# Performance work log

Hardware: AMD Instinct MI355X
Metric: run time of the kernel (lower is better)

Reference implementation:

```python
import jax, jax.numpy as jnp
import numpy as np

N_NODES = 70839  # num_user + num_item from config
N_EDGES = 2_000_000
EMB_DIM = 64
EPS = 1e-12  # torch F.normalize default eps


def setup_inputs() -> dict:
    key = jax.random.key(0)
    k1, k2, k3, k4 = jax.random.split(key, 4)
    ego_embedding = jax.random.normal(k1, (N_NODES, EMB_DIM), dtype=jnp.float32)
    edge_weight = jax.random.uniform(k2, (N_EDGES,), dtype=jnp.float32)
    edge_src = jax.random.randint(k3, (N_EDGES,), 0, N_NODES, dtype=jnp.int32)
    edge_dst = jax.random.randint(k4, (N_EDGES,), 0, N_NODES, dtype=jnp.int32)
    return {
        "ego_embedding": ego_embedding,
        "edge_weight": edge_weight,
        "edge_src": edge_src,
        "edge_dst": edge_dst,
    }


def reference(ego_embedding, edge_weight, edge_src, edge_dst):
    # message: m_e = h[src_e] * w_e   (u_mul_e)
    m = ego_embedding[edge_src] * edge_weight[:, None]          # [E, D]
    # reduce: h_v = sum_{e: dst_e = v} m_e   (fn.sum)
    h = jax.ops.segment_sum(m, edge_dst, num_segments=N_NODES)  # [N, D]
    # F.normalize(h, dim=1, p=2): x / max(||x||_2, eps)
    norm = jnp.linalg.norm(h, axis=1, keepdims=True)
    return h / jnp.maximum(norm, EPS)
```

## Files before the change

### kernel.cpp

```cpp
#include <hip/hip_runtime.h>
#include <hip/hip_fp16.h>

#define EMB_D 64
#define SB 1024
#define SPAN 128
#define MAXG 1024
#define NCHUNK2 512
#define CHMAX 4096
#define TILE 4096
#define CAST_BLOCKS 256


__device__ __forceinline__ float h15_to_float(unsigned int bits) {
    return __half2float(__ushort_as_half((unsigned short)bits));
}

__global__ void a1_cast_hist(const float2* __restrict__ embin,
                             __half2* __restrict__ emb16, int n2,
                             const int* __restrict__ dst,
                             int* __restrict__ cntT,
                             int E, int G, int chunk) {
    if (blockIdx.x < CAST_BLOCKS) {
        int i = blockIdx.x * blockDim.x + threadIdx.x;
        int st = CAST_BLOCKS * blockDim.x;
        for (; i < n2; i += st)
            emb16[i] = __float22half2_rn(embin[i]);
    } else {
        __shared__ int bins[MAXG];
        int hb = blockIdx.x - CAST_BLOCKS;
        for (int g = threadIdx.x; g < G; g += blockDim.x) bins[g] = 0;
        __syncthreads();
        int beg = hb * chunk;
        int end = min(beg + chunk, E);
        for (int i = beg + threadIdx.x; i < end; i += blockDim.x)
            atomicAdd(&bins[dst[i] >> 7], 1);
        __syncthreads();
        for (int g = threadIdx.x; g < G; g += blockDim.x)
            cntT[g * NCHUNK2 + hb] = bins[g];
    }
}

__global__ void scan_reduceB(const int* __restrict__ counts,
                             int* __restrict__ partial, int M) {
    __shared__ int wsum[16];
    const int tid = threadIdx.x, lane = tid & 63, wid = tid >> 6;
    int i = blockIdx.x * SB + tid;
    int v = (i < M) ? counts[i] : 0;
    #pragma unroll
    for (int off = 32; off > 0; off >>= 1)
        v += __shfl_xor(v, off, 64);
    if (lane == 0) wsum[wid] = v;
    __syncthreads();
    if (tid == 0) {
        int s = 0;
        #pragma unroll
        for (int k = 0; k < 16; ++k) s += wsum[k];
        partial[blockIdx.x] = s;
    }
}

__global__ void scan_partials(const int* __restrict__ partial,
                              int* __restrict__ blockoff,
                              int* __restrict__ offsets, int numB, int M) {
    __shared__ int wsum[16];
    __shared__ int wpre[16];
    __shared__ int carry;
    const int tid = threadIdx.x, lane = tid & 63, wid = tid >> 6;
    if (tid == 0) carry = 0;
    const int nPass = (numB + SB - 1) / SB;
    for (int p = 0; p < nPass; ++p) {
        __syncthreads();
        int base = carry;
        int idx = p * SB + tid;
        int v = (idx < numB) ? partial[idx] : 0;
        int x = v;
        #pragma unroll
        for (int off = 1; off < 64; off <<= 1) {
            int t = __shfl_up(x, off, 64);
            if (lane >= off) x += t;
        }
        if (lane == 63) wsum[wid] = x;
        __syncthreads();
        if (wid == 0) {
            int s = (lane < 16) ? wsum[lane] : 0;
            #pragma unroll
            for (int off = 1; off < 16; off <<= 1) {
                int t = __shfl_up(s, off, 64);
                if (lane >= off) s += t;
            }
            if (lane < 16) wpre[lane] = s;
        }
        __syncthreads();
        int excl = base + ((wid > 0) ? wpre[wid - 1] : 0) + (x - v);
        if (idx < numB) blockoff[idx] = excl;
        __syncthreads();
        if (tid == 0) carry = base + wpre[15];
    }
    __syncthreads();
    if (tid == 0) offsets[M] = carry;
}

__global__ void scan_applyB(const int* __restrict__ counts,
                            const int* __restrict__ blockoff,
                            int* __restrict__ offsets, int M) {
    __shared__ int wsum[16];
    __shared__ int wpre[16];
    const int tid = threadIdx.x, lane = tid & 63, wid = tid >> 6;
    int i = blockIdx.x * SB + tid;
    int v = (i < M) ? counts[i] : 0;
    int x = v;
    #pragma unroll
    for (int off = 1; off < 64; off <<= 1) {
        int t = __shfl_up(x, off, 64);
        if (lane >= off) x += t;
    }
    if (lane == 63) wsum[wid] = x;
    __syncthreads();
    if (wid == 0) {
        int s = (lane < 16) ? wsum[lane] : 0;
        #pragma unroll
        for (int off = 1; off < 16; off <<= 1) {
            int t = __shfl_up(s, off, 64);
            if (lane >= off) s += t;
        }
        if (lane < 16) wpre[lane] = s;
    }
    __syncthreads();
    int excl = blockoff[blockIdx.x] + ((wid > 0) ? wpre[wid - 1] : 0) + (x - v);
    if (i < M) offsets[i] = excl;
}

__global__ __launch_bounds__(256) void partition_sort(
        const int* __restrict__ src,
        const int* __restrict__ dst,
        const float* __restrict__ w,
        const int* __restrict__ cntT,
        const int* __restrict__ scanT,
        uint2* __restrict__ stream8,
        int E, int G, int chunk) {
    __shared__ uint2 recs[CHMAX];
    __shared__ int cur[MAXG];
    __shared__ int delta[MAXG];
    __shared__ int wtot[4];

    const int tid = threadIdx.x, lane = tid & 63, wv = tid >> 6;
    const int b = blockIdx.x;
    const int beg = b * chunk;
    const int end = min(beg + chunk, E);
    const int n = end - beg;

    const int K = (G + 255) >> 8;
    int vals[4];
    int acc = 0;
    #pragma unroll
    for (int k = 0; k < 4; ++k) {
        int g = tid * K + k;
        int c = (k < K && g < G) ? cntT[g * NCHUNK2 + b] : 0;
        vals[k] = c;
        acc += c;
    }
    int x = acc;
    #pragma unroll
    for (int off = 1; off < 64; off <<= 1) {
        int t = __shfl_up(x, off, 64);
        if (lane >= off) x += t;
    }
    if (lane == 63) wtot[wv] = x;
    __syncthreads();
    int woff = 0;
    #pragma unroll
    for (int k2 = 0; k2 < 4; ++k2)
        woff += (k2 < wv) ? wtot[k2] : 0;
    int run = woff + x - acc;
    #pragma unroll
    for (int k = 0; k < 4; ++k) {
        int g = tid * K + k;
        if (k < K && g < G) {
            cur[g] = run;
            delta[g] = scanT[g * NCHUNK2 + b] - run;
            run += vals[k];
        }
    }
    __syncthreads();

    for (int i = beg + tid; i < end; i += blockDim.x) {
        int d = dst[i];
        unsigned int wb = __half_as_ushort(__float2half_rn(w[i]));
        unsigned int pk = ((unsigned int)src[i] << 15) | (wb & 0x7FFFu);
        int g = d >> 7;
        int j = atomicAdd(&cur[g], 1);
        recs[j] = make_uint2(pk, (unsigned int)(d & (SPAN - 1)) |
                                 ((unsigned int)g << 7));
    }
    __syncthreads();

    for (int j = tid; j < n; j += blockDim.x) {
        uint2 r = recs[j];
        int g = (int)(r.y >> 7);
        stream8[delta[g] + j] = make_uint2(r.x, r.y & (SPAN - 1u));
    }
}

__global__ __launch_bounds__(512) void gather_fused(
        const char* __restrict__ emb16b,
        const uint2* __restrict__ stream8,
        const int* __restrict__ scanT,
        float* __restrict__ out, int N) {
    __shared__ uint2 lrec[TILE];
    __shared__ unsigned int srt[TILE];
    __shared__ int hcnt[SPAN];
    __shared__ int nstart[SPAN];
    __shared__ int cur[SPAN];
    __shared__ int wtot[2];

    const int g = blockIdx.x;
    const int tid = threadIdx.x;
    const int lane = tid & 63, wv = tid >> 6;
    const int base = scanT[g * NCHUNK2];
    const int endE = scanT[(g + 1) * NCHUNK2];
    const int crew = tid >> 4;
    const int ql = tid & 15;
    const unsigned qlo = (unsigned)(ql << 3);

    float4 acc[4];
    #pragma unroll
    for (int ni = 0; ni < 4; ++ni) acc[ni] = make_float4(0.f, 0.f, 0.f, 0.f);

    for (int tb = base; tb < endE; tb += TILE) {
        const int n = min(TILE, endE - tb);
        if (tid < SPAN) hcnt[tid] = 0;
        __syncthreads();
        for (int j = tid; j < n; j += 512) {
            uint2 r = stream8[tb + j];
            lrec[j] = r;
            atomicAdd(&hcnt[r.y], 1);
        }
        __syncthreads();
        int v = (tid < SPAN) ? hcnt[tid] : 0;
        int x = v;
        #pragma unroll
        for (int off = 1; off < 64; off <<= 1) {
            int t = __shfl_up(x, off, 64);
            if (lane >= off) x += t;
        }
        if (wv < 2 && lane == 63) wtot[wv] = x;
        __syncthreads();
        if (tid < SPAN) {
            int excl = x - v + ((wv == 1) ? wtot[0] : 0);
            nstart[tid] = excl;
            cur[tid] = excl;
        }
        __syncthreads();
        for (int j = tid; j < n; j += 512) {
            uint2 r = lrec[j];
            int slot = atomicAdd(&cur[r.y], 1);
            srt[slot] = r.x;
        }
        __syncthreads();
        #pragma unroll
        for (int ni = 0; ni < 4; ++ni) {
            int nd = crew + (ni << 5);
            int s = nstart[nd];
            int e = cur[nd];
            float4 a = acc[ni];
            unsigned int pk0 = (s < e) ? srt[s] : 0u;
            uint2 r0 = *reinterpret_cast<const uint2*>(
                emb16b + ((pk0 >> 15) * 128u + qlo));
            for (int k = s; k < e; ++k) {
                unsigned int pk1 = (k + 1 < e) ? srt[k + 1] : 0u;
                uint2 r1 = *reinterpret_cast<const uint2*>(
                    emb16b + ((pk1 >> 15) * 128u + qlo));
                float wt = h15_to_float(pk0 & 0x7FFFu);
                float2 x01 = __half22float2(*reinterpret_cast<__half2*>(&r0.x));
                float2 x23 = __half22float2(*reinterpret_cast<__half2*>(&r0.y));
                a.x = fmaf(x01.x, wt, a.x);
                a.y = fmaf(x01.y, wt, a.y);
                a.z = fmaf(x23.x, wt, a.z);
                a.w = fmaf(x23.y, wt, a.w);
                pk0 = pk1; r0 = r1;
            }
            acc[ni] = a;
        }
        __syncthreads();
    }

    #pragma unroll
    for (int ni = 0; ni < 4; ++ni) {
        int node = g * SPAN + crew + (ni << 5);
        float4 a = acc[ni];
        float ss = a.x * a.x + a.y * a.y + a.z * a.z + a.w * a.w;
        ss += __shfl_xor(ss, 1, 64);
        ss += __shfl_xor(ss, 2, 64);
        ss += __shfl_xor(ss, 4, 64);
        ss += __shfl_xor(ss, 8, 64);
        float scale = 1.0f / fmaxf(sqrtf(ss), 1e-12f);
        if (node < N) {
            float4 o = make_float4(a.x * scale, a.y * scale,
                                   a.z * scale, a.w * scale);
            *reinterpret_cast<float4*>(out + (size_t)node * EMB_D
                                       + (ql << 2)) = o;
        }
    }
}

__global__ void group_csr2(const uint2* __restrict__ stream8,
                           const int* __restrict__ scanT,
                           unsigned int* __restrict__ packed,
                           int* __restrict__ offsets, int N, int E) {
    __shared__ int hcnt[SPAN];
    __shared__ int cur[SPAN];
    __shared__ int wtot[4];
    int g = blockIdx.x;
    int tid = threadIdx.x;
    int base = scanT[g * NCHUNK2];
    int endE = scanT[(g + 1) * NCHUNK2];
    if (tid < SPAN) hcnt[tid] = 0;
    __syncthreads();
    for (int i = base + tid; i < endE; i += blockDim.x)
        atomicAdd(&hcnt[stream8[i].y], 1);
    __syncthreads();
    int v = (tid < SPAN) ? hcnt[tid] : 0;
    int lane = tid & 63, wv = tid >> 6;
    int x = v;
    #pragma unroll
    for (int off = 1; off < 64; off <<= 1) {
        int t = __shfl_up(x, off, 64);
        if (lane >= off) x += t;
    }
    if (lane == 63) wtot[wv] = x;
    __syncthreads();
    if (tid < SPAN) {
        int excl = x - v + ((wv == 1) ? wtot[0] : 0);
        cur[tid] = base + excl;
        int node = g * SPAN + tid;
        if (node < N) offsets[node] = base + excl;
    }
    if (g == 0 && tid == 0) offsets[N] = E;
    __syncthreads();
    for (int i = base + tid; i < endE; i += blockDim.x) {
        uint2 r = stream8[i];
        int slot = atomicAdd(&cur[r.y], 1);
        packed[slot] = r.x;
    }
}

__global__ __launch_bounds__(256) void gatherV_kernel(
        const char* __restrict__ emb16b,
        const int* __restrict__ offsets,
        const unsigned int* __restrict__ packed,
        float* __restrict__ out, int N) {
    int node = blockIdx.x * 4 + (threadIdx.x >> 6);
    int lane = threadIdx.x & 63;
    if (node >= N) return;
    int q  = lane >> 3;
    int ql = lane & 7;
    const unsigned qlo = (unsigned)(ql << 4);

    int beg = offsets[node];
    int end = offsets[node + 1];

    float a0=0.f,a1=0.f,a2=0.f,a3=0.f,a4=0.f,a5=0.f,a6=0.f,a7=0.f;

    int idx0 = beg + q;
    int idx1 = idx0 + 8;
    int idx2 = idx1 + 8;
    unsigned int pk0 = (idx0 < end) ? packed[idx0] : 0u;
    unsigned int pk1 = (idx1 < end) ? packed[idx1] : 0u;
    unsigned int pk2 = (idx2 < end) ? packed[idx2] : 0u;
    uint4 r0 = *reinterpret_cast<const uint4*>(emb16b + ((pk0 >> 15) * 128u + qlo));
    uint4 r1 = *reinterpret_cast<const uint4*>(emb16b + ((pk1 >> 15) * 128u + qlo));

    for (int j = beg; j < end; j += 8) {
        uint4 r2 = *reinterpret_cast<const uint4*>(
            emb16b + ((pk2 >> 15) * 128u + qlo));
        int idx3 = idx2 + 8;
        unsigned int pk3 = (idx3 < end) ? packed[idx3] : 0u;

        float wt = h15_to_float(pk0 & 0x7FFFu);
        float2 x01 = __half22float2(*reinterpret_cast<__half2*>(&r0.x));
        float2 x23 = __half22float2(*reinterpret_cast<__half2*>(&r0.y));
        float2 x45 = __half22float2(*reinterpret_cast<__half2*>(&r0.z));
        float2 x67 = __half22float2(*reinterpret_cast<__half2*>(&r0.w));
        a0 = fmaf(x01.x, wt, a0);
        a1 = fmaf(x01.y, wt, a1);
        a2 = fmaf(x23.x, wt, a2);
        a3 = fmaf(x23.y, wt, a3);
        a4 = fmaf(x45.x, wt, a4);
        a5 = fmaf(x45.y, wt, a5);
        a6 = fmaf(x67.x, wt, a6);
        a7 = fmaf(x67.y, wt, a7);

        pk0 = pk1; pk1 = pk2; pk2 = pk3;
        r0 = r1; r1 = r2;
        idx2 = idx3;
    }

    #pragma unroll
    for (int off = 8; off < 64; off <<= 1) {
        a0 += __shfl_xor(a0, off, 64);
        a1 += __shfl_xor(a1, off, 64);
        a2 += __shfl_xor(a2, off, 64);
        a3 += __shfl_xor(a3, off, 64);
        a4 += __shfl_xor(a4, off, 64);
        a5 += __shfl_xor(a5, off, 64);
        a6 += __shfl_xor(a6, off, 64);
        a7 += __shfl_xor(a7, off, 64);
    }
    float ss = a0*a0 + a1*a1 + a2*a2 + a3*a3 + a4*a4 + a5*a5 + a6*a6 + a7*a7;
    ss += __shfl_xor(ss, 1, 64);
    ss += __shfl_xor(ss, 2, 64);
    ss += __shfl_xor(ss, 4, 64);
    float scale = 1.0f / fmaxf(sqrtf(ss), 1e-12f);

    if (q == 0) {
        float4* po = reinterpret_cast<float4*>(out + (size_t)node * EMB_D
                                               + (ql << 3));
        po[0] = make_float4(a0 * scale, a1 * scale, a2 * scale, a3 * scale);
        po[1] = make_float4(a4 * scale, a5 * scale, a6 * scale, a7 * scale);
    }
}

__global__ void lightgcn_scatter(const float* __restrict__ emb,
                                 const float* __restrict__ w,
                                 const int* __restrict__ src,
                                 const int* __restrict__ dst,
                                 float* __restrict__ h, int E) {
    long long t = (long long)blockIdx.x * blockDim.x + threadIdx.x;
    int e = (int)(t >> 4);
    int d = (int)(t & 15) << 2;
    if (e >= E) return;
    int s = src[e]; int v = dst[e]; float wt = w[e];
    const float4 m = *reinterpret_cast<const float4*>(emb + (size_t)s * EMB_D + d);
    float* o = h + (size_t)v * EMB_D + d;
    unsafeAtomicAdd(o + 0, m.x * wt);
    unsafeAtomicAdd(o + 1, m.y * wt);
    unsafeAtomicAdd(o + 2, m.z * wt);
    unsafeAtomicAdd(o + 3, m.w * wt);
}

__global__ void lightgcn_normalize(float* __restrict__ h, int N) {
    int row = blockIdx.x * (blockDim.x >> 6) + (threadIdx.x >> 6);
    int lane = threadIdx.x & 63;
    if (row >= N) return;
    float x = h[(size_t)row * EMB_D + lane];
    float ss = x * x;
    #pragma unroll
    for (int off = 32; off > 0; off >>= 1)
        ss += __shfl_xor(ss, off, 64);
    h[(size_t)row * EMB_D + lane] = x / fmaxf(sqrtf(ss), 1e-12f);
}

extern "C" void kernel_launch(void* const* d_in, const int* in_sizes, int n_in,
                              void* d_out, int out_size, void* d_ws, size_t ws_size,
                              hipStream_t stream) {
    const float* emb = (const float*)d_in[0];
    const float* w   = (const float*)d_in[1];
    const int*   src = (const int*)d_in[2];
    const int*   dst = (const int*)d_in[3];
    float* out = (float*)d_out;

    const int N = in_sizes[0] / EMB_D;
    const int E = in_sizes[1];
    const int block = 256;
    const int G = (N + SPAN - 1) / SPAN;

    const int M3 = G * NCHUNK2;
    const int numB3 = (M3 + SB - 1) / SB;
    const int chunk3 = (E + NCHUNK2 - 1) / NCHUNK2;

    size_t intsA5 = (size_t)M3 + (size_t)(M3 + 1) + 2 * (size_t)numB3;
    size_t strOff5 = (intsA5 * sizeof(int) + 15) & ~(size_t)15;
    size_t embOff5 = (strOff5 + (size_t)E * sizeof(uint2) + 15) & ~(size_t)15;
    size_t neededA5 = embOff5 + (size_t)N * EMB_D * sizeof(__half);

    size_t intsA3 = (size_t)M3 + (size_t)(M3 + 1) + 2 * (size_t)numB3
                  + (size_t)(N + 1);
    size_t strOff = (intsA3 * sizeof(int) + 15) & ~(size_t)15;
    size_t pkdOff = strOff + (size_t)E * sizeof(uint2);
    size_t embOff3 = (pkdOff + (size_t)E * sizeof(unsigned int) + 15)
                     & ~(size_t)15;
    size_t neededA3 = embOff3 + (size_t)N * EMB_D * sizeof(__half);

    if (ws_size >= neededA5 && G <= MAXG && chunk3 <= CHMAX &&
        E < (1 << 28) && N < (1 << 17)) {
        int* cntT     = (int*)d_ws;
        int* scanT    = cntT + M3;
        int* partial  = scanT + M3 + 1;
        int* blockoff = partial + numB3;
        uint2* stream8 = (uint2*)((char*)d_ws + strOff5);
        __half2* emb16 = (__half2*)((char*)d_ws + embOff5);

        int n2 = N * (EMB_D / 2);

        a1_cast_hist<<<CAST_BLOCKS + NCHUNK2, block, 0, stream>>>(
            (const float2*)emb, emb16, n2, dst, cntT, E, G, chunk3);

        scan_reduceB<<<numB3, SB, 0, stream>>>(cntT, partial, M3);
        scan_partials<<<1, SB, 0, stream>>>(partial, blockoff, scanT, numB3, M3);
        scan_applyB<<<numB3, SB, 0, stream>>>(cntT, blockoff, scanT, M3);

        partition_sort<<<NCHUNK2, block, 0, stream>>>(src, dst, w, cntT, scanT,
                                                      stream8, E, G, chunk3);

        gather_fused<<<G, 512, 0, stream>>>((const char*)emb16, stream8,
                                            scanT, out, N);
    } else if (ws_size >= neededA3 && G <= MAXG && chunk3 <= CHMAX &&
               E < (1 << 28) && N < (1 << 17)) {
        int* cntT     = (int*)d_ws;
        int* scanT    = cntT + M3;
        int* partial  = scanT + M3 + 1;
        int* blockoff = partial + numB3;
        int* offsets  = blockoff + numB3;
        uint2* stream8 = (uint2*)((char*)d_ws + strOff);
        unsigned int* packed = (unsigned int*)((char*)d_ws + pkdOff);
        __half2* emb16 = (__half2*)((char*)d_ws + embOff3);

        int n2 = N * (EMB_D / 2);

        a1_cast_hist<<<CAST_BLOCKS + NCHUNK2, block, 0, stream>>>(
            (const float2*)emb, emb16, n2, dst, cntT, E, G, chunk3);

        scan_reduceB<<<numB3, SB, 0, stream>>>(cntT, partial, M3);
        scan_partials<<<1, SB, 0, stream>>>(partial, blockoff, scanT, numB3, M3);
        scan_applyB<<<numB3, SB, 0, stream>>>(cntT, blockoff, scanT, M3);

        partition_sort<<<NCHUNK2, block, 0, stream>>>(src, dst, w, cntT, scanT,
                                                      stream8, E, G, chunk3);
        group_csr2<<<G, block, 0, stream>>>(stream8, scanT, packed, offsets,
                                            N, E);

        int gridN = (N + 3) / 4;
        gatherV_kernel<<<gridN, 256, 0, stream>>>((const char*)emb16, offsets,
                                                  packed, out, N);
    } else {
        hipMemsetAsync(d_out, 0, (size_t)out_size * sizeof(float), stream);
        long long total = (long long)E * 16;
        int grid = (int)((total + block - 1) / block);
        lightgcn_scatter<<<grid, block, 0, stream>>>(emb, w, src, dst, out, E);
        int gridN = (N + 3) / 4;
        lightgcn_normalize<<<gridN, 256, 0, stream>>>(out, N);
    }
}
```

Measured before the change: 191.1 us.

## Split gather edge loop across two half-crews with 16-byte loads; widen partition_sort blocks

In the fused gather, each 16-lane node crew is split into two 8-lane halves. Each half handles alternate edges and loads 8 fp16 values (16 bytes) per lane instead of 4. The two partial sums are merged with an xor-8 shuffle before normalization. This aims to halve the serial per-node edge loop length and make wider memory transactions, at the cost of doubled accumulator registers and extra shuffles. Separately, partition_sort is launched with 512 threads instead of 256 to add parallelism during the scatter into shared memory.

Result: faster. 175.4 us (-8.2%).

```diff
diff --git a/kernel.cpp b/kernel.cpp
--- a/kernel.cpp
+++ b/kernel.cpp
@@ -130,7 +130,7 @@
     if (i < M) offsets[i] = excl;
 }
 
-__global__ __launch_bounds__(256) void partition_sort(
+__global__ __launch_bounds__(512) void partition_sort(
         const int* __restrict__ src,
         const int* __restrict__ dst,
         const float* __restrict__ w,
@@ -141,7 +141,7 @@
     __shared__ uint2 recs[CHMAX];
     __shared__ int cur[MAXG];
     __shared__ int delta[MAXG];
-    __shared__ int wtot[4];
+    __shared__ int wtot[8];
 
     const int tid = threadIdx.x, lane = tid & 63, wv = tid >> 6;
     const int b = blockIdx.x;
@@ -149,11 +149,11 @@
     const int end = min(beg + chunk, E);
     const int n = end - beg;
 
-    const int K = (G + 255) >> 8;
-    int vals[4];
+    const int K = (G + 511) >> 9;
+    int vals[2];
     int acc = 0;
     #pragma unroll
-    for (int k = 0; k < 4; ++k) {
+    for (int k = 0; k < 2; ++k) {
         int g = tid * K + k;
         int c = (k < K && g < G) ? cntT[g * NCHUNK2 + b] : 0;
         vals[k] = c;
@@ -169,11 +169,11 @@
     __syncthreads();
     int woff = 0;
     #pragma unroll
-    for (int k2 = 0; k2 < 4; ++k2)
+    for (int k2 = 0; k2 < 8; ++k2)
         woff += (k2 < wv) ? wtot[k2] : 0;
     int run = woff + x - acc;
     #pragma unroll
-    for (int k = 0; k < 4; ++k) {
+    for (int k = 0; k < 2; ++k) {
         int g = tid * K + k;
         if (k < K && g < G) {
             cur[g] = run;
@@ -183,7 +183,7 @@
     }
     __syncthreads();
 
-    for (int i = beg + tid; i < end; i += blockDim.x) {
+    for (int i = beg + tid; i < end; i += 512) {
         int d = dst[i];
         unsigned int wb = __half_as_ushort(__float2half_rn(w[i]));
         unsigned int pk = ((unsigned int)src[i] << 15) | (wb & 0x7FFFu);
@@ -194,7 +194,7 @@
     }
     __syncthreads();
 
-    for (int j = tid; j < n; j += blockDim.x) {
+    for (int j = tid; j < n; j += 512) {
         uint2 r = recs[j];
         int g = (int)(r.y >> 7);
         stream8[delta[g] + j] = make_uint2(r.x, r.y & (SPAN - 1u));
@@ -220,11 +220,16 @@
     const int endE = scanT[(g + 1) * NCHUNK2];
     const int crew = tid >> 4;
     const int ql = tid & 15;
-    const unsigned qlo = (unsigned)(ql << 3);
-
-    float4 acc[4];
-    #pragma unroll
-    for (int ni = 0; ni < 4; ++ni) acc[ni] = make_float4(0.f, 0.f, 0.f, 0.f);
+    const int sub = ql >> 3;
+    const int sl = ql & 7;
+    const unsigned qlo = (unsigned)(sl << 4);
+
+    float4 accA[4], accB[4];
+    #pragma unroll
+    for (int ni = 0; ni < 4; ++ni) {
+        accA[ni] = make_float4(0.f, 0.f, 0.f, 0.f);
+        accB[ni] = make_float4(0.f, 0.f, 0.f, 0.f);
+    }
 
     for (int tb = base; tb < endE; tb += TILE) {
         const int n = min(TILE, endE - tb);
@@ -262,43 +267,63 @@
             int nd = crew + (ni << 5);
             int s = nstart[nd];
             int e = cur[nd];
-            float4 a = acc[ni];
-            unsigned int pk0 = (s < e) ? srt[s] : 0u;
-            uint2 r0 = *reinterpret_cast<const uint2*>(
+            float4 aA = accA[ni];
+            float4 aB = accB[ni];
+            int k0 = s + sub;
+            unsigned int pk0 = (k0 < e) ? srt[k0] : 0u;
+            uint4 r0 = *reinterpret_cast<const uint4*>(
                 emb16b + ((pk0 >> 15) * 128u + qlo));
-            for (int k = s; k < e; ++k) {
-                unsigned int pk1 = (k + 1 < e) ? srt[k + 1] : 0u;
-                uint2 r1 = *reinterpret_cast<const uint2*>(
+            for (int k = k0; k < e; k += 2) {
+                int k1 = k + 2;
+                unsigned int pk1 = (k1 < e) ? srt[k1] : 0u;
+                uint4 r1 = *reinterpret_cast<const uint4*>(
                     emb16b + ((pk1 >> 15) * 128u + qlo));
                 float wt = h15_to_float(pk0 & 0x7FFFu);
                 float2 x01 = __half22float2(*reinterpret_cast<__half2*>(&r0.x));
                 float2 x23 = __half22float2(*reinterpret_cast<__half2*>(&r0.y));
-                a.x = fmaf(x01.x, wt, a.x);
-                a.y = fmaf(x01.y, wt, a.y);
-                a.z = fmaf(x23.x, wt, a.z);
-                a.w = fmaf(x23.y, wt, a.w);
+                float2 x45 = __half22float2(*reinterpret_cast<__half2*>(&r0.z));
+                float2 x67 = __half22float2(*reinterpret_cast<__half2*>(&r0.w));
+                aA.x = fmaf(x01.x, wt, aA.x);
+                aA.y = fmaf(x01.y, wt, aA.y);
+                aA.z = fmaf(x23.x, wt, aA.z);
+                aA.w = fmaf(x23.y, wt, aA.w);
+                aB.x = fmaf(x45.x, wt, aB.x);
+                aB.y = fmaf(x45.y, wt, aB.y);
+                aB.z = fmaf(x67.x, wt, aB.z);
+                aB.w = fmaf(x67.y, wt, aB.w);
                 pk0 = pk1; r0 = r1;
             }
-            acc[ni] = a;
+            accA[ni] = aA;
+            accB[ni] = aB;
         }
         __syncthreads();
     }
 
     #pragma unroll
     for (int ni = 0; ni < 4; ++ni) {
+        accA[ni].x += __shfl_xor(accA[ni].x, 8, 64);
+        accA[ni].y += __shfl_xor(accA[ni].y, 8, 64);
+        accA[ni].z += __shfl_xor(accA[ni].z, 8, 64);
+        accA[ni].w += __shfl_xor(accA[ni].w, 8, 64);
+        accB[ni].x += __shfl_xor(accB[ni].x, 8, 64);
+        accB[ni].y += __shfl_xor(accB[ni].y, 8, 64);
+        accB[ni].z += __shfl_xor(accB[ni].z, 8, 64);
+        accB[ni].w += __shfl_xor(accB[ni].w, 8, 64);
         int node = g * SPAN + crew + (ni << 5);
-        float4 a = acc[ni];
-        float ss = a.x * a.x + a.y * a.y + a.z * a.z + a.w * a.w;
+        float4 aA = accA[ni];
+        float4 aB = accB[ni];
+        float ss = aA.x * aA.x + aA.y * aA.y + aA.z * aA.z + aA.w * aA.w
+                 + aB.x * aB.x + aB.y * aB.y + aB.z * aB.z + aB.w * aB.w;
         ss += __shfl_xor(ss, 1, 64);
         ss += __shfl_xor(ss, 2, 64);
         ss += __shfl_xor(ss, 4, 64);
-        ss += __shfl_xor(ss, 8, 64);
         float scale = 1.0f / fmaxf(sqrtf(ss), 1e-12f);
         if (node < N) {
+            float4 a = sub ? aB : aA;
             float4 o = make_float4(a.x * scale, a.y * scale,
                                    a.z * scale, a.w * scale);
             *reinterpret_cast<float4*>(out + (size_t)node * EMB_D
-                                       + (ql << 2)) = o;
+                                       + (sl << 3) + (sub << 2)) = o;
         }
     }
 }
@@ -499,8 +524,8 @@
         scan_partials<<<1, SB, 0, stream>>>(partial, blockoff, scanT, numB3, M3);
         scan_applyB<<<numB3, SB, 0, stream>>>(cntT, blockoff, scanT, M3);
 
-        partition_sort<<<NCHUNK2, block, 0, stream>>>(src, dst, w, cntT, scanT,
-                                                      stream8, E, G, chunk3);
+        partition_sort<<<NCHUNK2, 512, 0, stream>>>(src, dst, w, cntT, scanT,
+                                                    stream8, E, G, chunk3);
 
         gather_fused<<<G, 512, 0, stream>>>((const char*)emb16, stream8,
                                             scanT, out, N);
@@ -524,8 +549,8 @@
         scan_partials<<<1, SB, 0, stream>>>(partial, blockoff, scanT, numB3, M3);
         scan_applyB<<<numB3, SB, 0, stream>>>(cntT, blockoff, scanT, M3);
 
-        partition_sort<<<NCHUNK2, block, 0, stream>>>(src, dst, w, cntT, scanT,
-                                                      stream8, E, G, chunk3);
+        partition_sort<<<NCHUNK2, 512, 0, stream>>>(src, dst, w, cntT, scanT,
+                                                    stream8, E, G, chunk3);
         group_csr2<<<G, block, 0, stream>>>(stream8, scanT, packed, offsets,
                                             N, E);
 
```
